# Kernel tuning notes

Hardware: AMD Instinct MI355X
Metric: run time of the kernel (lower is better)

## Reference

```python
import jax, jax.numpy as jnp
import numpy as np
from jax import lax

DIM = 256; RESO = 64; STRIPE = 8; NH = 8
HSP, WSP = RESO, STRIPE   # attention_mode=0: vertical stripes
HD = DIM // NH
B = 8; L = RESO * RESO
WIN = HSP * WSP           # tokens per window (512)


def _vertical_mask():
    # Faithful to verticalAttnMask: column labels 0/1/2 over last stripe, then
    # window-partition and pairwise-compare.
    shift = STRIPE // 2
    lab = np.zeros(RESO, np.float32)
    lab[RESO - STRIPE:RESO - shift] = 1.0
    lab[RESO - shift:] = 2.0
    img = np.broadcast_to(lab[None, :], (RESO, RESO))            # [H, W]
    # shiftedWindowVerticalPartition with reso=RESO, stripes=STRIPE
    mw = img.reshape(RESO, RESO // STRIPE, STRIPE).transpose(1, 0, 2).reshape(-1, WIN)
    diff = mw[:, None, :] - mw[:, :, None]                        # [nW, L, L]
    return jnp.asarray(np.where(diff != 0.0, -100.0, 0.0).astype(np.float32))

_MASK = _vertical_mask()  # [nW=8, 512, 512]


def _seq2cswin(x):
    Bx = x.shape[0]
    img = x.transpose(0, 2, 1).reshape(Bx, DIM, RESO, RESO)
    w = img.reshape(Bx, DIM, RESO // HSP, HSP, RESO // WSP, WSP)
    w = w.transpose(0, 2, 4, 3, 5, 1).reshape(-1, WIN, DIM)
    return w.reshape(-1, WIN, NH, HD).transpose(0, 2, 1, 3)


def _forward(qkv, scale, proj_w, proj_b, conv_w, conv_b):
    q, k, v = qkv[0], qkv[1], qkv[2]
    qw = _seq2cswin(q) * scale[0]
    kw = _seq2cswin(k)
    # get_lepe: window-partition v as images, depthwise 3x3 conv
    vimg = v.transpose(0, 2, 1).reshape(B, DIM, RESO, RESO)
    vwin = vimg.reshape(B, DIM, RESO // HSP, HSP, RESO // WSP, WSP)
    vwin = vwin.transpose(0, 2, 4, 1, 3, 5).reshape(-1, DIM, HSP, WSP)  # [B*nW, C, Hsp, Wsp]
    lepe = lax.conv_general_dilated(
        vwin, conv_w, (1, 1), ((1, 1), (1, 1)),
        dimension_numbers=('NCHW', 'OIHW', 'NCHW'), feature_group_count=DIM
    ) + conv_b[None, :, None, None]
    lepe = lepe.reshape(-1, NH, HD, WIN).transpose(0, 1, 3, 2)
    vw = vwin.reshape(-1, NH, HD, WIN).transpose(0, 1, 3, 2)
    attn = jnp.einsum('wnid,wnjd->wnij', qw, kw)
    # currentDepth odd, mode 0 -> vertical shifted-window mask
    attn = attn + jnp.tile(_MASK, (B, 1, 1))[:, None, :, :]
    attn = jax.nn.softmax(attn, axis=-1)
    x = jnp.einsum('wnij,wnjd->wnid', attn, vw) + lepe
    x = x.transpose(0, 2, 1, 3).reshape(-1, WIN, DIM)
    x = x @ proj_w.T + proj_b
    # CSwin2img then flatten back to [B, L, C]
    x = x.reshape(B, RESO // HSP, RESO // WSP, HSP, WSP, DIM)
    x = x.transpose(0, 1, 3, 2, 4, 5).reshape(B, RESO, RESO, DIM)
    return x.reshape(B, L, DIM)


def setup_inputs() -> dict:
    key = jax.random.key(0)
    ks = jax.random.split(key, 5)
    qkv = jax.random.normal(ks[0], (3, B, L, DIM), jnp.float32)
    scale = jnp.full((1,), HD ** (-0.5), jnp.float32)
    proj_w = jax.random.normal(ks[1], (DIM, DIM), jnp.float32) * (DIM ** -0.5)
    proj_b = jax.random.normal(ks[2], (DIM,), jnp.float32) * 0.02
    conv_w = jax.random.normal(ks[3], (DIM, 1, 3, 3), jnp.float32) * 0.1
    conv_b = jax.random.normal(ks[4], (DIM,), jnp.float32) * 0.02
    return {"qkv": qkv, "scale": scale, "proj_w": proj_w, "proj_b": proj_b,
            "conv_w": conv_w, "conv_b": conv_b}


def reference(qkv, scale, proj_w, proj_b, conv_w, conv_b):
    return _forward(qkv, scale, proj_w, proj_b, conv_w, conv_b)
```

## Files before the change

### kernel.cpp

```cpp
#include <hip/hip_runtime.h>
#include <hip/hip_bf16.h>

#define BATCH 8
#define NH    8
#define HD    32
#define WIN   512
#define DIM   256
#define RESO  64
#define SEQL  4096
#define VSTRIDE 520
#define WPAD  264

#define LOG2E 1.44269504088896340736f

extern "C" __device__ float __ocml_native_exp2_f32(float);

typedef __attribute__((ext_vector_type(8))) short short8;
typedef __attribute__((ext_vector_type(4))) float floatx4;

__device__ __forceinline__ unsigned short f2bf(float f) {
    union { float f; unsigned int i; } x; x.f = f;
    unsigned int r = x.i + 0x7fff + ((x.i >> 16) & 1);
    return (unsigned short)(r >> 16);
}
__device__ __forceinline__ float bf2f(unsigned short u) {
    union { unsigned int i; float f; } x; x.i = ((unsigned int)u) << 16; return x.f;
}
__device__ __forceinline__ unsigned int pk2(float lo, float hi) {
    return ((unsigned int)f2bf(hi) << 16) | (unsigned int)f2bf(lo);
}
__device__ __forceinline__ unsigned int pk2t(float lo, float hi) {
    union { float f; unsigned int i; } a, b; a.f = lo; b.f = hi;
    return __builtin_amdgcn_perm(b.i, a.i, 0x07060302);
}

union FragU {
    unsigned int  u[4];
    unsigned short us[8];
    short8        s;
    ushort4       v4[2];
};

__global__ __launch_bounds__(512, 4)
void attn_mfma_kernel(const float* __restrict__ qkv,
                      const float* __restrict__ scale_p,
                      const float* __restrict__ conv_w,
                      const float* __restrict__ conv_b,
                      unsigned short* __restrict__ X)
{
    __shared__ alignas(16) unsigned short Klds[WIN * HD];
    __shared__ alignas(16) unsigned short Vt[HD * VSTRIDE];
    __shared__ float cw[HD * 9];
    __shared__ float cb[HD];

    const int wh_raw = blockIdx.x;
    const int wh   = ((wh_raw & 7) << 6) | (wh_raw >> 3);
    const int bw   = wh >> 3;
    const int head = wh & 7;
    const int b    = bw >> 3;
    const int wx   = bw & 7;
    const int tid  = threadIdx.x;

    const float scale = scale_p[0] * LOG2E;
    const size_t plane = (size_t)BATCH * SEQL * DIM;
    const float* qg = qkv;
    const float* kg = qkv + plane;
    const float* vg = qkv + 2 * plane;

    #pragma unroll
    for (int kk = 0; kk < 4; ++kk) {
        const int idx = tid + kk * 512;
        const int t = idx >> 2, c8 = idx & 3;
        const size_t goff = ((size_t)b * SEQL + (size_t)(t >> 3) * RESO + wx * 8 + (t & 7)) * DIM
                          + head * HD + c8 * 8;
        const float4 k0 = *(const float4*)(kg + goff);
        const float4 k1 = *(const float4*)(kg + goff + 4);
        uint4 pk;
        pk.x = pk2t(k0.x, k0.y); pk.y = pk2t(k0.z, k0.w);
        pk.z = pk2t(k1.x, k1.y); pk.w = pk2t(k1.z, k1.w);
        const int p = c8 ^ ((t >> 1) & 3);
        *(uint4*)&Klds[t * HD + p * 8] = pk;
    }
    #pragma unroll
    for (int kk = 0; kk < 16; ++kk) {
        const int idx = tid + kk * 512;
        const int ch = idx & 31, tp = idx >> 5;
        const int t = tp * 2;
        const size_t goff = ((size_t)b * SEQL + (size_t)(t >> 3) * RESO + wx * 8 + (t & 7)) * DIM
                          + head * HD + ch;
        const float v0 = vg[goff];
        const float v1 = vg[goff + DIM];
        *(unsigned int*)&Vt[ch * VSTRIDE + t] = pk2(v0, v1);
    }
    if (tid < HD * 9) cw[tid] = conv_w[head * HD * 9 + tid];
    if (tid < HD)     cb[tid] = conv_b[head * HD + tid];

    const int lane = tid & 63, wid = tid >> 6;
    const int q4 = lane >> 4, nn = lane & 15;
    const int qbase = wid * 64;
    const bool mwin = (wx == 7);

    short8 qf[4];
    #pragma unroll
    for (int qq = 0; qq < 4; ++qq) {
        const int t = qbase + qq * 16 + nn;
        const size_t goff = ((size_t)b * SEQL + (size_t)(t >> 3) * RESO + wx * 8 + (t & 7)) * DIM
                          + head * HD + q4 * 8;
        const float4 a = *(const float4*)(qg + goff);
        const float4 c = *(const float4*)(qg + goff + 4);
        FragU f;
        f.u[0] = pk2t(a.x * scale, a.y * scale);
        f.u[1] = pk2t(a.z * scale, a.w * scale);
        f.u[2] = pk2t(c.x * scale, c.y * scale);
        f.u[3] = pk2t(c.z * scale, c.w * scale);
        qf[qq] = f.s;
    }
    __syncthreads();

    float mk[4];
    #pragma unroll
    for (int r = 0; r < 4; ++r) {
        const bool kgrp = (((q4 * 4 + r) & 7) < 4);
        const bool qgrp = ((nn & 7) < 4);
        mk[r] = (kgrp != qgrp) ? (-100.f * LOG2E) : 0.f;
    }

    floatx4 acc[4][2];
    #pragma unroll
    for (int qq = 0; qq < 4; ++qq) {
        acc[qq][0] = (floatx4){0.f, 0.f, 0.f, 0.f};
        acc[qq][1] = (floatx4){0.f, 0.f, 0.f, 0.f};
    }
    float rs[4] = {0.f, 0.f, 0.f, 0.f};
    const floatx4 zf = (floatx4){0.f, 0.f, 0.f, 0.f};

    const int kswz = (q4 ^ ((nn >> 1) & 3)) * 8;
    const unsigned short* kp0 = &Klds[nn * HD + kswz];
    const unsigned short* kp1 = &Klds[(16 + nn) * HD + kswz];
    const unsigned short* vp0 = &Vt[nn * VSTRIDE + q4 * 4];
    const unsigned short* vp1 = &Vt[(16 + nn) * VSTRIDE + q4 * 4];

    short8 kf0 = *(const short8*)kp0;
    short8 kf1 = *(const short8*)kp1;
    short8 vf0, vf1;
    {
        FragU f0, f1;
        f0.v4[0] = *(const ushort4*)vp0;
        f0.v4[1] = *(const ushort4*)(vp0 + 16);
        f1.v4[0] = *(const ushort4*)vp1;
        f1.v4[1] = *(const ushort4*)(vp1 + 16);
        vf0 = f0.s; vf1 = f1.s;
    }

    for (int kc = 0; kc < 16; ++kc) {
        const int nko = ((kc + 1) & 15) * 32;
        short8 nkf0 = *(const short8*)(kp0 + nko * HD);
        short8 nkf1 = *(const short8*)(kp1 + nko * HD);
        short8 nvf0, nvf1;
        {
            FragU f0, f1;
            f0.v4[0] = *(const ushort4*)(vp0 + nko);
            f0.v4[1] = *(const ushort4*)(vp0 + nko + 16);
            f1.v4[0] = *(const ushort4*)(vp1 + nko);
            f1.v4[1] = *(const ushort4*)(vp1 + nko + 16);
            nvf0 = f0.s; nvf1 = f1.s;
        }

        __builtin_amdgcn_s_setprio(1);
        #pragma unroll
        for (int qq = 0; qq < 4; ++qq) {
            floatx4 s0 = __builtin_amdgcn_mfma_f32_16x16x32_bf16(kf0, qf[qq], zf, 0, 0, 0);
            floatx4 s1 = __builtin_amdgcn_mfma_f32_16x16x32_bf16(kf1, qf[qq], zf, 0, 0, 0);
            if (mwin) {
                #pragma unroll
                for (int r = 0; r < 4; ++r) { s0[r] += mk[r]; s1[r] += mk[r]; }
            }
            float p[8];
            #pragma unroll
            for (int r = 0; r < 4; ++r) {
                p[r]     = __ocml_native_exp2_f32(s0[r]);
                p[4 + r] = __ocml_native_exp2_f32(s1[r]);
            }
            rs[qq] += ((p[0] + p[1]) + (p[2] + p[3])) + ((p[4] + p[5]) + (p[6] + p[7]));
            FragU pf;
            pf.u[0] = pk2t(p[0], p[1]);
            pf.u[1] = pk2t(p[2], p[3]);
            pf.u[2] = pk2t(p[4], p[5]);
            pf.u[3] = pk2t(p[6], p[7]);
            acc[qq][0] = __builtin_amdgcn_mfma_f32_16x16x32_bf16(vf0, pf.s, acc[qq][0], 0, 0, 0);
            acc[qq][1] = __builtin_amdgcn_mfma_f32_16x16x32_bf16(vf1, pf.s, acc[qq][1], 0, 0, 0);
        }
        __builtin_amdgcn_s_setprio(0);

        kf0 = nkf0; kf1 = nkf1; vf0 = nvf0; vf1 = nvf1;
    }

    float inv[4];
    #pragma unroll
    for (int qq = 0; qq < 4; ++qq) {
        float v = rs[qq];
        v += __shfl_xor(v, 16);
        v += __shfl_xor(v, 32);
        inv[qq] = 1.0f / v;
    }

    #pragma unroll
    for (int qq = 0; qq < 4; ++qq) {
        const int t = qbase + qq * 16 + nn;
        const int h = t >> 3, wi = t & 7;
        #pragma unroll
        for (int nt = 0; nt < 2; ++nt) {
            const int chb = nt * 16 + q4 * 4;
            float o[4];
            #pragma unroll
            for (int r = 0; r < 4; ++r)
                o[r] = acc[qq][nt][r] * inv[qq] + cb[chb + r];
            #pragma unroll
            for (int dh = -1; dh <= 1; ++dh) {
                const int hh = h + dh;
                if (hh < 0 || hh >= RESO) continue;
                #pragma unroll
                for (int dw = -1; dw <= 1; ++dw) {
                    const int ww = wi + dw;
                    if (ww < 0 || ww >= 8) continue;
                    const int tj  = hh * 8 + ww;
                    const int wof = (dh + 1) * 3 + (dw + 1);
                    #pragma unroll
                    for (int r = 0; r < 4; ++r)
                        o[r] += cw[(chb + r) * 9 + wof] * bf2f(Vt[(chb + r) * VSTRIDE + tj]);
                }
            }
            ushort4 st;
            st.x = f2bf(o[0]); st.y = f2bf(o[1]); st.z = f2bf(o[2]); st.w = f2bf(o[3]);
            *(ushort4*)&X[((size_t)bw * WIN + t) * DIM + head * HD + chb] = st;
        }
    }
}

__global__ __launch_bounds__(256, 4)
void proj_mfma_kernel(const unsigned short* __restrict__ X,
                      const float* __restrict__ pw,
                      const float* __restrict__ pb,
                      float* __restrict__ out)
{
    __shared__ alignas(16) unsigned short Wl[64 * WPAD];

    const int raw  = blockIdx.x;
    const int bx   = ((raw & 7) << 7) | (raw >> 3);
    const int mchk = bx >> 2;
    const int nblk = bx & 3;
    const int tid  = threadIdx.x;
    const int n0   = nblk * 64;

    {
        const int row = tid >> 2;
        const int cb0 = (tid & 3) * 64;
        #pragma unroll
        for (int c = 0; c < 64; c += 8) {
            const float4 w0 = *(const float4*)&pw[(size_t)(n0 + row) * DIM + cb0 + c];
            const float4 w1 = *(const float4*)&pw[(size_t)(n0 + row) * DIM + cb0 + c + 4];
            uint4 pk;
            pk.x = pk2(w0.x, w0.y); pk.y = pk2(w0.z, w0.w);
            pk.z = pk2(w1.x, w1.y); pk.w = pk2(w1.z, w1.w);
            *(uint4*)&Wl[row * WPAD + cb0 + c] = pk;
        }
    }
    __syncthreads();

    const int lane = tid & 63, wid = tid >> 6;
    const int q4 = lane >> 4, nn = lane & 15;
    const int m0 = mchk * 128 + wid * 32;

    floatx4 acc[4][2];
    #pragma unroll
    for (int i = 0; i < 4; ++i)
        #pragma unroll
        for (int j = 0; j < 2; ++j)
            acc[i][j] = (floatx4){0.f, 0.f, 0.f, 0.f};

    for (int kk = 0; kk < 8; ++kk) {
        short8 af[4], bf[2];
        #pragma unroll
        for (int nt = 0; nt < 4; ++nt)
            af[nt] = *(const short8*)&Wl[(nt * 16 + nn) * WPAD + kk * 32 + q4 * 8];
        #pragma unroll
        for (int mt = 0; mt < 2; ++mt) {
            const int m = m0 + mt * 16 + nn;
            bf[mt] = *(const short8*)&X[(size_t)m * DIM + kk * 32 + q4 * 8];
        }
        #pragma unroll
        for (int nt = 0; nt < 4; ++nt)
            #pragma unroll
            for (int mt = 0; mt < 2; ++mt)
                acc[nt][mt] = __builtin_amdgcn_mfma_f32_16x16x32_bf16(af[nt], bf[mt], acc[nt][mt], 0, 0, 0);
    }

    float4 bias[4];
    #pragma unroll
    for (int nt = 0; nt < 4; ++nt)
        bias[nt] = *(const float4*)&pb[n0 + nt * 16 + q4 * 4];

    size_t rowoff[2];
    #pragma unroll
    for (int mt = 0; mt < 2; ++mt) {
        const int m  = m0 + mt * 16 + nn;
        const int bw = m >> 9, t = m & 511;
        const int bb = bw >> 3, wx = bw & 7, hh = t >> 3, wi = t & 7;
        rowoff[mt] = ((size_t)bb * SEQL + (size_t)hh * RESO + wx * 8 + wi) * DIM;
    }

    #pragma unroll
    for (int nt = 0; nt < 4; ++nt)
        #pragma unroll
        for (int mt = 0; mt < 2; ++mt) {
            float4 v;
            v.x = acc[nt][mt][0] + bias[nt].x;
            v.y = acc[nt][mt][1] + bias[nt].y;
            v.z = acc[nt][mt][2] + bias[nt].z;
            v.w = acc[nt][mt][3] + bias[nt].w;
            *(float4*)&out[rowoff[mt] + n0 + nt * 16 + q4 * 4] = v;
        }
}

extern "C" void kernel_launch(void* const* d_in, const int* in_sizes, int n_in,
                              void* d_out, int out_size, void* d_ws, size_t ws_size,
                              hipStream_t stream)
{
    const float* qkv    = (const float*)d_in[0];
    const float* scale  = (const float*)d_in[1];
    const float* proj_w = (const float*)d_in[2];
    const float* proj_b = (const float*)d_in[3];
    const float* conv_w = (const float*)d_in[4];
    const float* conv_b = (const float*)d_in[5];

    unsigned short* X = (unsigned short*)d_ws;

    attn_mfma_kernel<<<dim3(BATCH * NH * 8), dim3(512), 0, stream>>>(
        qkv, scale, conv_w, conv_b, X);

    proj_mfma_kernel<<<dim3(1024), dim3(256), 0, stream>>>(
        X, proj_w, proj_b, (float*)d_out);
}
```

Before: 214.1 us.

## Split attention query rows across two blocks and stream K from global

Doubles the attention grid so each block handles half of a window's 512 query rows, with each wave owning 32 rows instead of 64. K is no longer staged into LDS; each wave loads its K fragments straight from global memory every iteration and converts them to bf16 in registers. The V transpose into LDS is now done twice per window/head, once by each of the two blocks. The register prefetch of K/V fragments across iterations is removed. The aim is more blocks for occupancy and less LDS, at the cost of redundant global K/V reads and exposed K load latency inside the loop.

```diff
diff --git a/kernel.cpp b/kernel.cpp
--- a/kernel.cpp
+++ b/kernel.cpp
@@ -48,13 +48,14 @@
                       const float* __restrict__ conv_b,
                       unsigned short* __restrict__ X)
 {
-    __shared__ alignas(16) unsigned short Klds[WIN * HD];
     __shared__ alignas(16) unsigned short Vt[HD * VSTRIDE];
     __shared__ float cw[HD * 9];
     __shared__ float cb[HD];
 
-    const int wh_raw = blockIdx.x;
-    const int wh   = ((wh_raw & 7) << 6) | (wh_raw >> 3);
+    const int raw  = blockIdx.x;
+    const int wh2  = ((raw & 7) << 7) | (raw >> 3);
+    const int wh   = wh2 >> 1;
+    const int qhalf= wh2 & 1;
     const int bw   = wh >> 3;
     const int head = wh & 7;
     const int b    = bw >> 3;
@@ -67,20 +68,6 @@
     const float* kg = qkv + plane;
     const float* vg = qkv + 2 * plane;
 
-    #pragma unroll
-    for (int kk = 0; kk < 4; ++kk) {
-        const int idx = tid + kk * 512;
-        const int t = idx >> 2, c8 = idx & 3;
-        const size_t goff = ((size_t)b * SEQL + (size_t)(t >> 3) * RESO + wx * 8 + (t & 7)) * DIM
-                          + head * HD + c8 * 8;
-        const float4 k0 = *(const float4*)(kg + goff);
-        const float4 k1 = *(const float4*)(kg + goff + 4);
-        uint4 pk;
-        pk.x = pk2t(k0.x, k0.y); pk.y = pk2t(k0.z, k0.w);
-        pk.z = pk2t(k1.x, k1.y); pk.w = pk2t(k1.z, k1.w);
-        const int p = c8 ^ ((t >> 1) & 3);
-        *(uint4*)&Klds[t * HD + p * 8] = pk;
-    }
     #pragma unroll
     for (int kk = 0; kk < 16; ++kk) {
         const int idx = tid + kk * 512;
@@ -97,12 +84,12 @@
 
     const int lane = tid & 63, wid = tid >> 6;
     const int q4 = lane >> 4, nn = lane & 15;
-    const int qbase = wid * 64;
+    const int qbase = qhalf * 256 + wid * 32;
     const bool mwin = (wx == 7);
 
-    short8 qf[4];
-    #pragma unroll
-    for (int qq = 0; qq < 4; ++qq) {
+    short8 qf[2];
+    #pragma unroll
+    for (int qq = 0; qq < 2; ++qq) {
         const int t = qbase + qq * 16 + nn;
         const size_t goff = ((size_t)b * SEQL + (size_t)(t >> 3) * RESO + wx * 8 + (t & 7)) * DIM
                           + head * HD + q4 * 8;
@@ -125,52 +112,49 @@
         mk[r] = (kgrp != qgrp) ? (-100.f * LOG2E) : 0.f;
     }
 
-    floatx4 acc[4][2];
-    #pragma unroll
-    for (int qq = 0; qq < 4; ++qq) {
+    floatx4 acc[2][2];
+    #pragma unroll
+    for (int qq = 0; qq < 2; ++qq) {
         acc[qq][0] = (floatx4){0.f, 0.f, 0.f, 0.f};
         acc[qq][1] = (floatx4){0.f, 0.f, 0.f, 0.f};
     }
-    float rs[4] = {0.f, 0.f, 0.f, 0.f};
+    float rs[2] = {0.f, 0.f};
     const floatx4 zf = (floatx4){0.f, 0.f, 0.f, 0.f};
 
-    const int kswz = (q4 ^ ((nn >> 1) & 3)) * 8;
-    const unsigned short* kp0 = &Klds[nn * HD + kswz];
-    const unsigned short* kp1 = &Klds[(16 + nn) * HD + kswz];
+    const float* kptr = kg + ((size_t)b * SEQL + (size_t)(nn >> 3) * RESO + wx * 8 + (nn & 7)) * DIM
+                           + head * HD + q4 * 8;
+    const int JSTEP = 2 * RESO * DIM;
     const unsigned short* vp0 = &Vt[nn * VSTRIDE + q4 * 4];
     const unsigned short* vp1 = &Vt[(16 + nn) * VSTRIDE + q4 * 4];
 
-    short8 kf0 = *(const short8*)kp0;
-    short8 kf1 = *(const short8*)kp1;
-    short8 vf0, vf1;
-    {
-        FragU f0, f1;
-        f0.v4[0] = *(const ushort4*)vp0;
-        f0.v4[1] = *(const ushort4*)(vp0 + 16);
-        f1.v4[0] = *(const ushort4*)vp1;
-        f1.v4[1] = *(const ushort4*)(vp1 + 16);
-        vf0 = f0.s; vf1 = f1.s;
-    }
-
     for (int kc = 0; kc < 16; ++kc) {
-        const int nko = ((kc + 1) & 15) * 32;
-        short8 nkf0 = *(const short8*)(kp0 + nko * HD);
-        short8 nkf1 = *(const short8*)(kp1 + nko * HD);
-        short8 nvf0, nvf1;
+        const float4 a0 = *(const float4*)(kptr);
+        const float4 c0 = *(const float4*)(kptr + 4);
+        const float4 a1 = *(const float4*)(kptr + JSTEP);
+        const float4 c1 = *(const float4*)(kptr + JSTEP + 4);
+        kptr += 2 * JSTEP;
+        FragU kf0, kf1;
+        kf0.u[0] = pk2t(a0.x, a0.y); kf0.u[1] = pk2t(a0.z, a0.w);
+        kf0.u[2] = pk2t(c0.x, c0.y); kf0.u[3] = pk2t(c0.z, c0.w);
+        kf1.u[0] = pk2t(a1.x, a1.y); kf1.u[1] = pk2t(a1.z, a1.w);
+        kf1.u[2] = pk2t(c1.x, c1.y); kf1.u[3] = pk2t(c1.z, c1.w);
+
+        const int ko = kc * 32;
+        short8 vf0, vf1;
         {
             FragU f0, f1;
-            f0.v4[0] = *(const ushort4*)(vp0 + nko);
-            f0.v4[1] = *(const ushort4*)(vp0 + nko + 16);
-            f1.v4[0] = *(const ushort4*)(vp1 + nko);
-            f1.v4[1] = *(const ushort4*)(vp1 + nko + 16);
-            nvf0 = f0.s; nvf1 = f1.s;
+            f0.v4[0] = *(const ushort4*)(vp0 + ko);
+            f0.v4[1] = *(const ushort4*)(vp0 + ko + 16);
+            f1.v4[0] = *(const ushort4*)(vp1 + ko);
+            f1.v4[1] = *(const ushort4*)(vp1 + ko + 16);
+            vf0 = f0.s; vf1 = f1.s;
         }
 
         __builtin_amdgcn_s_setprio(1);
         #pragma unroll
-        for (int qq = 0; qq < 4; ++qq) {
-            floatx4 s0 = __builtin_amdgcn_mfma_f32_16x16x32_bf16(kf0, qf[qq], zf, 0, 0, 0);
-            floatx4 s1 = __builtin_amdgcn_mfma_f32_16x16x32_bf16(kf1, qf[qq], zf, 0, 0, 0);
+        for (int qq = 0; qq < 2; ++qq) {
+            floatx4 s0 = __builtin_amdgcn_mfma_f32_16x16x32_bf16(kf0.s, qf[qq], zf, 0, 0, 0);
+            floatx4 s1 = __builtin_amdgcn_mfma_f32_16x16x32_bf16(kf1.s, qf[qq], zf, 0, 0, 0);
             if (mwin) {
                 #pragma unroll
                 for (int r = 0; r < 4; ++r) { s0[r] += mk[r]; s1[r] += mk[r]; }
@@ -191,13 +175,11 @@
             acc[qq][1] = __builtin_amdgcn_mfma_f32_16x16x32_bf16(vf1, pf.s, acc[qq][1], 0, 0, 0);
         }
         __builtin_amdgcn_s_setprio(0);
-
-        kf0 = nkf0; kf1 = nkf1; vf0 = nvf0; vf1 = nvf1;
-    }
-
-    float inv[4];
-    #pragma unroll
-    for (int qq = 0; qq < 4; ++qq) {
+    }
+
+    float inv[2];
+    #pragma unroll
+    for (int qq = 0; qq < 2; ++qq) {
         float v = rs[qq];
         v += __shfl_xor(v, 16);
         v += __shfl_xor(v, 32);
@@ -205,7 +187,7 @@
     }
 
     #pragma unroll
-    for (int qq = 0; qq < 4; ++qq) {
+    for (int qq = 0; qq < 2; ++qq) {
         const int t = qbase + qq * 16 + nn;
         const int h = t >> 3, wi = t & 7;
         #pragma unroll
@@ -335,7 +317,7 @@
 
     unsigned short* X = (unsigned short*)d_ws;
 
-    attn_mfma_kernel<<<dim3(BATCH * NH * 8), dim3(512), 0, stream>>>(
+    attn_mfma_kernel<<<dim3(BATCH * NH * 8 * 2), dim3(512), 0, stream>>>(
         qkv, scale, conv_w, conv_b, X);
 
     proj_mfma_kernel<<<dim3(1024), dim3(256), 0, stream>>>(
```

After: 366.7 us. +71.3%, slower.
